# Kernel tuning notes

Hardware: AMD Instinct MI355X
Metric: run time of the kernel (lower is better)

## Reference

```python
import jax, jax.numpy as jnp
import numpy as np

LN_EPS = 1e-5


def _pos_embed_2d(w, h, c, dtype=jnp.float32):
    # matches build_2d_sincos_position_embedding: meshgrid indexing='xy' -> (h, w) grids
    grid_w = jnp.arange(w, dtype=jnp.float32)
    grid_h = jnp.arange(h, dtype=jnp.float32)
    gw, gh = jnp.meshgrid(grid_w, grid_h, indexing='xy')  # each (h, w)
    pos_dim = c // 4
    omega = 1.0 / (10000.0 ** (jnp.arange(pos_dim, dtype=jnp.float32) / pos_dim))
    out_w = gw.reshape(-1, 1) * omega[None]  # (h*w, pos_dim)
    out_h = gh.reshape(-1, 1) * omega[None]
    pe = jnp.concatenate([jnp.sin(out_w), jnp.cos(out_w), jnp.sin(out_h), jnp.cos(out_h)], axis=1)
    return pe.astype(dtype)  # (h*w, c)


def setup_inputs() -> dict:
    key = jax.random.key(0)
    k1, k2 = jax.random.split(key)
    N, C, H, W = 16, 256, 40, 40
    x = jax.random.normal(k1, (N, C, H, W), dtype=jnp.float32)
    ln_w = jnp.ones((C,), dtype=jnp.float32)
    ln_b = jnp.zeros((C,), dtype=jnp.float32)
    qkv_w = jax.random.normal(k2, (3 * C, C), dtype=jnp.float32) * 0.02  # 1x1 conv weight
    qkv_b = jnp.zeros((3 * C,), dtype=jnp.float32)
    gamma = jnp.ones((1,), dtype=jnp.float32)
    return {"x": x, "ln_w": ln_w, "ln_b": ln_b, "qkv_w": qkv_w, "qkv_b": qkv_b, "gamma": gamma}


def reference(x, ln_w, ln_b, qkv_w, qkv_b, gamma):
    N, C, H, W = x.shape
    scale = C ** (-0.5)
    identity = x

    # LayerNorm over channels (computed in NHWC like the torch permute dance)
    xh = jnp.transpose(x, (0, 2, 3, 1))  # (N, H, W, C)
    mu = jnp.mean(xh, axis=-1, keepdims=True)
    var = jnp.mean(jnp.square(xh - mu), axis=-1, keepdims=True)
    xn = (xh - mu) * jax.lax.rsqrt(var + LN_EPS) * ln_w + ln_b

    # 1x1 conv == per-pixel linear
    qkv = jnp.einsum('nhwc,oc->nhwo', xn, qkv_w) + qkv_b  # (N, H, W, 3C)
    qkv = qkv.reshape(N, H * W, 3 * C)
    q, k, v = jnp.split(qkv, 3, axis=-1)  # each (N, HW, C)

    pe = _pos_embed_2d(W, H, C, x.dtype)  # (HW, C)
    q = q + pe
    k = k + pe

    attn = jax.nn.softmax(jnp.einsum('nqc,nkc->nqk', q, k) * scale, axis=-1)
    out = jnp.einsum('nqk,nkc->nqc', attn, v)  # (N, HW, C)
    out = jnp.transpose(out, (0, 2, 1)).reshape(N, C, H, W)
    return identity + gamma[0] * out
```

## Files before the change

kernel.cpp:

```cpp
#include <hip/hip_runtime.h>
#include <hip/hip_bf16.h>

typedef float f32x4 __attribute__((ext_vector_type(4)));
typedef float f32x16 __attribute__((ext_vector_type(16)));
typedef __bf16 v8bf __attribute__((ext_vector_type(8)));
typedef unsigned short ushortx4 __attribute__((ext_vector_type(4)));
typedef unsigned short ushortx8 __attribute__((ext_vector_type(8)));
typedef unsigned int uint4v __attribute__((ext_vector_type(4)));

#define NIMG 16
#define CCH  256
#define HWP  1600
#define APIT 264

__device__ __forceinline__ unsigned short f2bf(float f) {
  unsigned int u = __builtin_bit_cast(unsigned int, f);
  u = (u + 0x7FFFu + ((u >> 16) & 1u)) >> 16;
  return (unsigned short)u;
}

__device__ __forceinline__ f32x4 mfma16(v8bf a, v8bf b, f32x4 c) {
  return __builtin_amdgcn_mfma_f32_16x16x32_bf16(a, b, c, 0, 0, 0);
}

__device__ __forceinline__ unsigned cvtpk(float a, float b) {
  unsigned r;
  asm("v_cvt_pk_bf16_f32 %0, %1, %2" : "=v"(r) : "v"(a), "v"(b));
  return r;
}
#define PSWAP(a, b) asm("v_permlane32_swap_b32 %0, %1" : "+v"(a), "+v"(b))

__global__ void prep_kernel(const float* __restrict__ qkv_w,
                            float* __restrict__ pe,
                            unsigned short* __restrict__ w_frag) {
  int tid = blockIdx.x * blockDim.x + threadIdx.x;
  int nthr = gridDim.x * blockDim.x;
  for (int i = tid; i < 768 * 256; i += nthr) {
    int o = i >> 8, c = i & 255;
    int tile = o >> 4, lr = o & 15;
    int ks = c >> 5, lg = (c >> 3) & 3, e = c & 7;
    w_frag[(((size_t)tile * 8 + ks) * 64 + lg * 16 + lr) * 8 + e] = f2bf(qkv_w[i]);
  }
  const float c1 = 9.210340371976184f / 64.f;
  for (int i = tid; i < HWP * 256; i += nthr) {
    int p = i >> 8, c = i & 255;
    int j = p % 40, ii = p / 40;
    int tt = c & 63;
    float omega = expf(-(float)tt * c1);
    float coord = (c < 128) ? (float)j : (float)ii;
    float a = coord * omega;
    pe[i] = ((c & 64) == 0) ? sinf(a) : cosf(a);
  }
}

__global__ __launch_bounds__(512, 4) void ln_qkv_kernel(
    const float* __restrict__ x, const float* __restrict__ ln_w, const float* __restrict__ ln_b,
    const unsigned short* __restrict__ w_frag, const float* __restrict__ qkv_b,
    const float* __restrict__ pe,
    unsigned short* __restrict__ q_arr, unsigned short* __restrict__ k_arr,
    unsigned short* __restrict__ v_arr) {
  __shared__ unsigned short buf[64][APIT];
  __shared__ float red_s[8][64], red_q[8][64];
  __shared__ float mu_s[64], rs_s[64];

  int t = threadIdx.x;
  int n = blockIdx.x / 25, pt = blockIdx.x % 25;
  int pix0 = pt * 64;
  int p = t & 63, g = t >> 6;
  const float* xb = x + (size_t)n * CCH * HWP + pix0;

  {
    float sum = 0.f, sq = 0.f;
#pragma unroll
    for (int i = 0; i < 32; ++i) {
      float v = xb[(size_t)(g * 32 + i) * HWP + p];
      sum += v; sq += v * v;
    }
    red_s[g][p] = sum; red_q[g][p] = sq;
  }
  __syncthreads();
  if (t < 64) {
    float s = 0.f, q2 = 0.f;
#pragma unroll
    for (int gg = 0; gg < 8; ++gg) { s += red_s[gg][t]; q2 += red_q[gg][t]; }
    float mu = s * (1.f / 256.f);
    float var = q2 * (1.f / 256.f) - mu * mu;
    mu_s[t] = mu;
    rs_s[t] = rsqrtf(var + 1e-5f);
  }
  __syncthreads();
  {
    float mu = mu_s[p], rs = rs_s[p];
#pragma unroll
    for (int i4 = 0; i4 < 8; ++i4) {
      int c0 = g * 32 + i4 * 4;
      f32x4 lw = *(const f32x4*)&ln_w[c0];
      f32x4 lb = *(const f32x4*)&ln_b[c0];
      ushortx4 pk;
#pragma unroll
      for (int r = 0; r < 4; ++r) {
        float v = xb[(size_t)(c0 + r) * HWP + p];
        pk[r] = f2bf((v - mu) * rs * lw[r] + lb[r]);
      }
      *(ushortx4*)&buf[p][c0] = pk;
    }
  }
  __syncthreads();

  int w = t >> 6, l = t & 63, lr = l & 15, lg = l >> 4;
  f32x4 acc[6][4];
#pragma unroll
  for (int nf = 0; nf < 6; ++nf)
#pragma unroll
    for (int mi = 0; mi < 4; ++mi) acc[nf][mi] = (f32x4){0.f, 0.f, 0.f, 0.f};

#pragma unroll
  for (int ks = 0; ks < 8; ++ks) {
    v8bf bF[4];
#pragma unroll
    for (int mi = 0; mi < 4; ++mi)
      bF[mi] = *(const v8bf*)&buf[mi * 16 + lr][ks * 32 + lg * 8];
#pragma unroll
    for (int nf = 0; nf < 6; ++nf) {
      int tile = w + nf * 8;
      v8bf wf = *(const v8bf*)&w_frag[(((size_t)tile * 8 + ks) * 64 + l) * 8];
#pragma unroll
      for (int mi = 0; mi < 4; ++mi) acc[nf][mi] = mfma16(wf, bF[mi], acc[nf][mi]);
    }
  }

  int lgh = lg >> 1, lgl = lg & 1;
#pragma unroll
  for (int nf = 0; nf < 2; ++nf) {
    int tile = w + nf * 8;
    f32x4 bi = *(const f32x4*)&qkv_b[tile * 16 + lg * 4];
#pragma unroll
    for (int mi = 0; mi < 4; ++mi) {
      int pix = pix0 + mi * 16 + lr;
      f32x4 pev = *(const f32x4*)&pe[(size_t)pix * 256 + tile * 16 + lg * 4];
      f32x4 vv = (acc[nf][mi] + bi + pev) * 0.0625f;
      ushortx4 pk = {f2bf(vv[0]), f2bf(vv[1]), f2bf(vv[2]), f2bf(vv[3])};
      int qt = pix >> 5, l31 = pix & 31;
      size_t ad = ((((size_t)n * 50 + qt) * 16 + tile) * 2 + lgh) * 256 + l31 * 8 + lgl * 4;
      *(ushortx4*)&q_arr[ad] = pk;
    }
  }
#pragma unroll
  for (int nf = 2; nf < 4; ++nf) {
    int tile = w + nf * 8;
    int dt = tile - 16;
    f32x4 bi = *(const f32x4*)&qkv_b[tile * 16 + lg * 4];
#pragma unroll
    for (int mi = 0; mi < 4; ++mi) {
      int pix = pix0 + mi * 16 + lr;
      f32x4 pev = *(const f32x4*)&pe[(size_t)pix * 256 + dt * 16 + lg * 4];
      f32x4 vv = acc[nf][mi] + bi + pev;
      ushortx4 pk = {f2bf(vv[0]), f2bf(vv[1]), f2bf(vv[2]), f2bf(vv[3])};
      size_t ad = (((size_t)n * 16 + dt) * 1600 + pix) * 16 + lgh * 8 + lgl * 4;
      *(ushortx4*)&k_arr[ad] = pk;
    }
  }
#pragma unroll
  for (int nf = 4; nf < 6; ++nf) {
    int tile = w + nf * 8;
    f32x4 bi = *(const f32x4*)&qkv_b[tile * 16 + lg * 4];
#pragma unroll
    for (int mi = 0; mi < 4; ++mi) {
      int pix = pix0 + mi * 16 + lr;
      int kvs = pix >> 4, hi = (pix >> 3) & 1, e = pix & 7;
      f32x4 vv = acc[nf][mi] + bi;
      size_t vb = (((size_t)n * 100 + kvs) * 2 + hi) * 2048 + e;
      int d0 = (tile - 32) * 16 + lg * 4;
#pragma unroll
      for (int r = 0; r < 4; ++r)
        v_arr[vb + (size_t)(d0 + r) * 8] = f2bf(vv[r]);
    }
  }
}

__global__ __launch_bounds__(256, 2) void attn_kernel(
    const unsigned short* __restrict__ q_arr, const unsigned short* __restrict__ k_arr,
    const unsigned short* __restrict__ v_arr, const float* __restrict__ x,
    const float* __restrict__ gamma, float* __restrict__ out) {
  __shared__ float sx[2][2][2][4][64][4];

  int t = threadIdx.x;
  int wv = t >> 6, l = t & 63;
  int l31 = l & 31, hi = l >> 5;
  int qsub = wv & 1, dh = wv >> 1;
  int dto = dh * 8;
  int dto32 = dh * 4;
  int slot = blockIdx.x & 7, j = blockIdx.x >> 3;
  int n = slot + 8 * (j / 25);
  int qb = j % 25;
  int qt = qb * 2 + qsub;
  int q0 = qt * 32;

  v8bf qf[8];
  {
    const unsigned short* qp = q_arr + (((size_t)n * 50 + qt) * 32 + hi) * 256 + l31 * 8;
#pragma unroll
    for (int i = 0; i < 8; ++i)
      qf[i] = *(const v8bf*)(qp + (dto + i) * 512);
  }

  f32x16 acc[4];
#pragma unroll
  for (int dd = 0; dd < 4; ++dd)
#pragma unroll
    for (int r = 0; r < 16; ++r) acc[dd][r] = 0.f;

  float m_run = -1e30f, l_run = 0.f;

  const unsigned short* kbase = k_arr + (size_t)n * (16 * 1600 * 16) +
                                (size_t)dto * 25600 + hi * 8;
  const unsigned short* vbase = v_arr + (size_t)n * (100 * 2 * 256 * 8) +
                                hi * 2048 + l31 * 8 + dto32 * 256;

  v8bf kc[8];
#pragma unroll
  for (int i = 0; i < 8; ++i)
    kc[i] = *(const v8bf*)(kbase + (size_t)i * 25600 + l31 * 16);

  for (int kt = 0; kt < 50; ++kt) {
    int pb = kt & 1;
    int ktn = (kt + 1 < 50) ? kt + 1 : 0;

    f32x16 s0, s1;
#pragma unroll
    for (int r = 0; r < 16; ++r) { s0[r] = 0.f; s1[r] = 0.f; }
#pragma unroll
    for (int i = 0; i < 8; i += 2) {
      s0 = __builtin_amdgcn_mfma_f32_32x32x16_bf16(kc[i], qf[i], s0, 0, 0, 0);
      s1 = __builtin_amdgcn_mfma_f32_32x32x16_bf16(kc[i + 1], qf[i + 1], s1, 0, 0, 0);
    }
#pragma unroll
    for (int i = 0; i < 8; ++i)
      kc[i] = *(const v8bf*)(kbase + (size_t)i * 25600 + (ktn * 32 + l31) * 16);

#pragma unroll
    for (int r4 = 0; r4 < 4; ++r4) {
      f32x4 vv = {s0[r4 * 4 + 0] + s1[r4 * 4 + 0], s0[r4 * 4 + 1] + s1[r4 * 4 + 1],
                  s0[r4 * 4 + 2] + s1[r4 * 4 + 2], s0[r4 * 4 + 3] + s1[r4 * 4 + 3]};
      *(f32x4*)&sx[qsub][pb][dh][r4][l][0] = vv;
    }

    v8bf vf0[4], vf1[4];
    {
      const unsigned short* vp = vbase + (size_t)kt * 8192;
#pragma unroll
      for (int i = 0; i < 4; ++i) vf0[i] = *(const v8bf*)(vp + i * 256);
#pragma unroll
      for (int i = 0; i < 4; ++i) vf1[i] = *(const v8bf*)(vp + 4096 + i * 256);
    }

    __syncthreads();

    float p[16];
#pragma unroll
    for (int r4 = 0; r4 < 4; ++r4) {
      f32x4 oth = *(const f32x4*)&sx[qsub][pb][dh ^ 1][r4][l][0];
#pragma unroll
      for (int rr = 0; rr < 4; ++rr)
        p[r4 * 4 + rr] = (s0[r4 * 4 + rr] + s1[r4 * 4 + rr]) + oth[rr];
    }

    float t0 = fmaxf(p[0], p[1]), t1 = fmaxf(p[2], p[3]);
    float t2 = fmaxf(p[4], p[5]), t3 = fmaxf(p[6], p[7]);
    float t4 = fmaxf(p[8], p[9]), t5 = fmaxf(p[10], p[11]);
    float t6 = fmaxf(p[12], p[13]), t7 = fmaxf(p[14], p[15]);
    float mx = fmaxf(fmaxf(fmaxf(t0, t1), fmaxf(t2, t3)),
                     fmaxf(fmaxf(t4, t5), fmaxf(t6, t7)));
    mx = fmaxf(mx, __shfl_xor(mx, 32));
    if (!__all(mx <= m_run + 2.f)) {
      float mnew = fmaxf(m_run, mx);
      float alpha = __expf(m_run - mnew);
      l_run *= alpha;
#pragma unroll
      for (int dd = 0; dd < 4; ++dd)
#pragma unroll
        for (int r = 0; r < 16; ++r) acc[dd][r] *= alpha;
      m_run = mnew;
    }
#pragma unroll
    for (int r = 0; r < 16; ++r) p[r] = __expf(p[r] - m_run);
    float sA = (p[0] + p[1]) + (p[2] + p[3]);
    float sB = (p[4] + p[5]) + (p[6] + p[7]);
    float sC = (p[8] + p[9]) + (p[10] + p[11]);
    float sD = (p[12] + p[13]) + (p[14] + p[15]);
    float sum = (sA + sB) + (sC + sD);
    sum += __shfl_xor(sum, 32);
    l_run += sum;

    unsigned x0 = cvtpk(p[0], p[1]), x1 = cvtpk(p[2], p[3]);
    unsigned y0 = cvtpk(p[4], p[5]), y1 = cvtpk(p[6], p[7]);
    PSWAP(x0, y0); PSWAP(x1, y1);
    uint4v u0 = {x0, x1, y0, y1};
    v8bf pf0 = __builtin_bit_cast(v8bf, u0);
    unsigned z0 = cvtpk(p[8], p[9]), z1 = cvtpk(p[10], p[11]);
    unsigned w0 = cvtpk(p[12], p[13]), w1 = cvtpk(p[14], p[15]);
    PSWAP(z0, w0); PSWAP(z1, w1);
    uint4v u1 = {z0, z1, w0, w1};
    v8bf pf1 = __builtin_bit_cast(v8bf, u1);

#pragma unroll
    for (int dd = 0; dd < 4; ++dd) {
      acc[dd] = __builtin_amdgcn_mfma_f32_32x32x16_bf16(vf0[dd], pf0, acc[dd], 0, 0, 0);
      acc[dd] = __builtin_amdgcn_mfma_f32_32x32x16_bf16(vf1[dd], pf1, acc[dd], 0, 0, 0);
    }
  }

  float inv = 1.f / l_run;
  float gm = gamma[0];
#pragma unroll
  for (int dd = 0; dd < 4; ++dd) {
#pragma unroll
    for (int r = 0; r < 16; ++r) {
      int d = (dto32 + dd) * 32 + (r & 3) + 8 * (r >> 2) + 4 * hi;
      size_t base = ((size_t)n * 256 + d) * HWP + q0 + l31;
      out[base] = x[base] + gm * acc[dd][r] * inv;
    }
  }
}

extern "C" void kernel_launch(void* const* d_in, const int* in_sizes, int n_in,
                              void* d_out, int out_size, void* d_ws, size_t ws_size,
                              hipStream_t stream) {
  const float* x     = (const float*)d_in[0];
  const float* ln_w  = (const float*)d_in[1];
  const float* ln_b  = (const float*)d_in[2];
  const float* qkv_w = (const float*)d_in[3];
  const float* qkv_b = (const float*)d_in[4];
  const float* gamma = (const float*)d_in[5];
  float* out = (float*)d_out;

  char* ws = (char*)d_ws;
  unsigned short* w_frag = (unsigned short*)ws;
  float*          pe     = (float*)(ws + 393216);
  unsigned short* q_arr  = (unsigned short*)(ws + 2031616);
  unsigned short* k_arr  = (unsigned short*)(ws + 15138816);
  unsigned short* v_arr  = (unsigned short*)(ws + 28246016);

  hipLaunchKernelGGL(prep_kernel, dim3(384), dim3(256), 0, stream, qkv_w, pe, w_frag);
  hipLaunchKernelGGL(ln_qkv_kernel, dim3(400), dim3(512), 0, stream,
                     x, ln_w, ln_b, w_frag, qkv_b, pe, q_arr, k_arr, v_arr);
  hipLaunchKernelGGL(attn_kernel, dim3(400), dim3(256), 0, stream,
                     q_arr, k_arr, v_arr, x, gamma, out);
}
```

Before: 133.0 us.

## Split attention KV range across wave pairs with flash-decoding style merge

Each attention block now handles one 32-query tile instead of two, with the two wave pairs processing disjoint halves of the key/value sequence. Partial softmax statistics and accumulators are merged through shared memory at the end. The grid doubles to 800 blocks to raise occupancy across the CUs. The cost is an extra LDS reduction and twice the Q fragment loads per query.

```diff
diff --git a/kernel.cpp b/kernel.cpp
--- a/kernel.cpp
+++ b/kernel.cpp
@@ -182,19 +182,20 @@
     const unsigned short* __restrict__ q_arr, const unsigned short* __restrict__ k_arr,
     const unsigned short* __restrict__ v_arr, const float* __restrict__ x,
     const float* __restrict__ gamma, float* __restrict__ out) {
-  __shared__ float sx[2][2][2][4][64][4];
+  __shared__ float pool[8192];
+  __shared__ float mls[4][2][32];
 
   int t = threadIdx.x;
   int wv = t >> 6, l = t & 63;
   int l31 = l & 31, hi = l >> 5;
-  int qsub = wv & 1, dh = wv >> 1;
+  int kvh = wv & 1, dh = wv >> 1;
   int dto = dh * 8;
   int dto32 = dh * 4;
   int slot = blockIdx.x & 7, j = blockIdx.x >> 3;
-  int n = slot + 8 * (j / 25);
-  int qb = j % 25;
-  int qt = qb * 2 + qsub;
+  int n = slot + 8 * (j / 50);
+  int qt = j % 50;
   int q0 = qt * 32;
+  int kt0 = kvh * 25;
 
   v8bf qf[8];
   {
@@ -220,11 +221,12 @@
   v8bf kc[8];
 #pragma unroll
   for (int i = 0; i < 8; ++i)
-    kc[i] = *(const v8bf*)(kbase + (size_t)i * 25600 + l31 * 16);
-
-  for (int kt = 0; kt < 50; ++kt) {
-    int pb = kt & 1;
-    int ktn = (kt + 1 < 50) ? kt + 1 : 0;
+    kc[i] = *(const v8bf*)(kbase + (size_t)i * 25600 + (kt0 * 32 + l31) * 16);
+
+  for (int it = 0; it < 25; ++it) {
+    int kt = kt0 + it;
+    int pb = it & 1;
+    int ktn = (it + 1 < 25) ? kt + 1 : kt0;
 
     f32x16 s0, s1;
 #pragma unroll
@@ -238,11 +240,12 @@
     for (int i = 0; i < 8; ++i)
       kc[i] = *(const v8bf*)(kbase + (size_t)i * 25600 + (ktn * 32 + l31) * 16);
 
+    int sxw = ((pb * 2 + kvh) * 2 + dh) * 1024;
 #pragma unroll
     for (int r4 = 0; r4 < 4; ++r4) {
       f32x4 vv = {s0[r4 * 4 + 0] + s1[r4 * 4 + 0], s0[r4 * 4 + 1] + s1[r4 * 4 + 1],
                   s0[r4 * 4 + 2] + s1[r4 * 4 + 2], s0[r4 * 4 + 3] + s1[r4 * 4 + 3]};
-      *(f32x4*)&sx[qsub][pb][dh][r4][l][0] = vv;
+      *(f32x4*)&pool[sxw + r4 * 256 + l * 4] = vv;
     }
 
     v8bf vf0[4], vf1[4];
@@ -256,10 +259,11 @@
 
     __syncthreads();
 
+    int sxr = ((pb * 2 + kvh) * 2 + (dh ^ 1)) * 1024;
     float p[16];
 #pragma unroll
     for (int r4 = 0; r4 < 4; ++r4) {
-      f32x4 oth = *(const f32x4*)&sx[qsub][pb][dh ^ 1][r4][l][0];
+      f32x4 oth = *(const f32x4*)&pool[sxr + r4 * 256 + l * 4];
 #pragma unroll
       for (int rr = 0; rr < 4; ++rr)
         p[r4 * 4 + rr] = (s0[r4 * 4 + rr] + s1[r4 * 4 + rr]) + oth[rr];
@@ -310,17 +314,55 @@
     }
   }
 
-  float inv = 1.f / l_run;
+  __syncthreads();
+  if (hi == 0) {
+    mls[kvh * 2 + dh][0][l31] = m_run;
+    mls[kvh * 2 + dh][1][l31] = l_run;
+  }
+  if (kvh == 0) {
+#pragma unroll
+    for (int r4 = 0; r4 < 4; ++r4) {
+      f32x4 a2 = {acc[2][r4 * 4 + 0], acc[2][r4 * 4 + 1], acc[2][r4 * 4 + 2], acc[2][r4 * 4 + 3]};
+      f32x4 a3 = {acc[3][r4 * 4 + 0], acc[3][r4 * 4 + 1], acc[3][r4 * 4 + 2], acc[3][r4 * 4 + 3]};
+      *(f32x4*)&pool[(((dh * 2 + 0) * 2 + 0) * 4 + r4) * 256 + l * 4] = a2;
+      *(f32x4*)&pool[(((dh * 2 + 0) * 2 + 1) * 4 + r4) * 256 + l * 4] = a3;
+    }
+  } else {
+#pragma unroll
+    for (int r4 = 0; r4 < 4; ++r4) {
+      f32x4 a0 = {acc[0][r4 * 4 + 0], acc[0][r4 * 4 + 1], acc[0][r4 * 4 + 2], acc[0][r4 * 4 + 3]};
+      f32x4 a1 = {acc[1][r4 * 4 + 0], acc[1][r4 * 4 + 1], acc[1][r4 * 4 + 2], acc[1][r4 * 4 + 3]};
+      *(f32x4*)&pool[(((dh * 2 + 1) * 2 + 0) * 4 + r4) * 256 + l * 4] = a0;
+      *(f32x4*)&pool[(((dh * 2 + 1) * 2 + 1) * 4 + r4) * 256 + l * 4] = a1;
+    }
+  }
+  __syncthreads();
+
+  float m_o = mls[(kvh ^ 1) * 2 + dh][0][l31];
+  float l_o = mls[(kvh ^ 1) * 2 + dh][1][l31];
+  float M = fmaxf(m_run, m_o);
+  float a_s = __expf(m_run - M), a_o = __expf(m_o - M);
+  float linv = 1.f / (l_run * a_s + l_o * a_o);
   float gm = gamma[0];
-#pragma unroll
-  for (int dd = 0; dd < 4; ++dd) {
-#pragma unroll
-    for (int r = 0; r < 16; ++r) {
-      int d = (dto32 + dd) * 32 + (r & 3) + 8 * (r >> 2) + 4 * hi;
-      size_t base = ((size_t)n * 256 + d) * HWP + q0 + l31;
-      out[base] = x[base] + gm * acc[dd][r] * inv;
-    }
-  }
+
+#define FIN(DT, PK, S)                                                          \
+  {                                                                             \
+    _Pragma("unroll")                                                           \
+    for (int r4 = 0; r4 < 4; ++r4) {                                            \
+      f32x4 oth = *(const f32x4*)&pool[(((dh * 2 + (PK)) * 2 + (S)) * 4 + r4) * 256 + l * 4]; \
+      _Pragma("unroll")                                                         \
+      for (int rr = 0; rr < 4; ++rr) {                                          \
+        int r = r4 * 4 + rr;                                                    \
+        float o = acc[DT][r] * a_s + oth[rr] * a_o;                             \
+        int d = (dto32 + (DT)) * 32 + (r & 3) + 8 * (r >> 2) + 4 * hi;          \
+        size_t base = ((size_t)n * 256 + d) * HWP + q0 + l31;                   \
+        out[base] = x[base] + gm * o * linv;                                    \
+      }                                                                         \
+    }                                                                           \
+  }
+  if (kvh == 0) { FIN(0, 1, 0); FIN(1, 1, 1); }
+  else          { FIN(2, 0, 0); FIN(3, 0, 1); }
+#undef FIN
 }
 
 extern "C" void kernel_launch(void* const* d_in, const int* in_sizes, int n_in,
@@ -344,6 +386,6 @@
   hipLaunchKernelGGL(prep_kernel, dim3(384), dim3(256), 0, stream, qkv_w, pe, w_frag);
   hipLaunchKernelGGL(ln_qkv_kernel, dim3(400), dim3(512), 0, stream,
                      x, ln_w, ln_b, w_frag, qkv_b, pe, q_arr, k_arr, v_arr);
-  hipLaunchKernelGGL(attn_kernel, dim3(400), dim3(256), 0, stream,
+  hipLaunchKernelGGL(attn_kernel, dim3(800), dim3(256), 0, stream,
                      q_arr, k_arr, v_arr, x, gamma, out);
 }
```

Result: no change. 135.6 us (+2.0%).

## Split attention into single-wave blocks, use exp2 softmax, stage V stores through LDS

Applied to the files above, without the earlier changes.

The attention kernel now gives each 64-thread block a full 256-dim QK^T dot product. The old version split the head dimension across waves and exchanged partial scores through shared memory with a barrier every key tile; that exchange is removed. Q is prescaled by log2(e)/16 so the softmax can use the raw v_exp_f32 instruction, and the rescale-deferral threshold is adjusted to match. The V output in the LN/QKV kernel is first transposed in LDS and then written with 16-byte stores instead of scattered 2-byte stores. The cost is twice the K and Q register footprint per wave, and each K tile is now loaded redundantly by two blocks.

```diff
diff --git a/kernel.cpp b/kernel.cpp
--- a/kernel.cpp
+++ b/kernel.cpp
@@ -13,6 +13,9 @@
 #define HWP  1600
 #define APIT 264
 
+#define QSCALE 0.09016844f
+#define DEFER_THR 2.885390f
+
 __device__ __forceinline__ unsigned short f2bf(float f) {
   unsigned int u = __builtin_bit_cast(unsigned int, f);
   u = (u + 0x7FFFu + ((u >> 16) & 1u)) >> 16;
@@ -26,6 +29,11 @@
 __device__ __forceinline__ unsigned cvtpk(float a, float b) {
   unsigned r;
   asm("v_cvt_pk_bf16_f32 %0, %1, %2" : "=v"(r) : "v"(a), "v"(b));
+  return r;
+}
+__device__ __forceinline__ float exp2v(float x) {
+  float r;
+  asm("v_exp_f32 %0, %1" : "=v"(r) : "v"(x));
   return r;
 }
 #define PSWAP(a, b) asm("v_permlane32_swap_b32 %0, %1" : "+v"(a), "+v"(b))
@@ -128,8 +136,22 @@
       for (int mi = 0; mi < 4; ++mi) acc[nf][mi] = mfma16(wf, bF[mi], acc[nf][mi]);
     }
   }
+  __syncthreads();
 
   int lgh = lg >> 1, lgl = lg & 1;
+#pragma unroll
+  for (int nf = 4; nf < 6; ++nf) {
+    int tile = w + nf * 8;
+    f32x4 bi = *(const f32x4*)&qkv_b[tile * 16 + lg * 4];
+    int d0 = (tile - 32) * 16 + lg * 4;
+#pragma unroll
+    for (int mi = 0; mi < 4; ++mi) {
+      int pixl = mi * 16 + lr;
+      f32x4 vv = acc[nf][mi] + bi;
+      ushortx4 pk = {f2bf(vv[0]), f2bf(vv[1]), f2bf(vv[2]), f2bf(vv[3])};
+      *(ushortx4*)&buf[pixl][d0] = pk;
+    }
+  }
 #pragma unroll
   for (int nf = 0; nf < 2; ++nf) {
     int tile = w + nf * 8;
@@ -138,7 +160,7 @@
     for (int mi = 0; mi < 4; ++mi) {
       int pix = pix0 + mi * 16 + lr;
       f32x4 pev = *(const f32x4*)&pe[(size_t)pix * 256 + tile * 16 + lg * 4];
-      f32x4 vv = (acc[nf][mi] + bi + pev) * 0.0625f;
+      f32x4 vv = (acc[nf][mi] + bi + pev) * QSCALE;
       ushortx4 pk = {f2bf(vv[0]), f2bf(vv[1]), f2bf(vv[2]), f2bf(vv[3])};
       int qt = pix >> 5, l31 = pix & 31;
       size_t ad = ((((size_t)n * 50 + qt) * 16 + tile) * 2 + lgh) * 256 + l31 * 8 + lgl * 4;
@@ -160,48 +182,39 @@
       *(ushortx4*)&k_arr[ad] = pk;
     }
   }
-#pragma unroll
-  for (int nf = 4; nf < 6; ++nf) {
-    int tile = w + nf * 8;
-    f32x4 bi = *(const f32x4*)&qkv_b[tile * 16 + lg * 4];
-#pragma unroll
-    for (int mi = 0; mi < 4; ++mi) {
-      int pix = pix0 + mi * 16 + lr;
-      int kvs = pix >> 4, hi = (pix >> 3) & 1, e = pix & 7;
-      f32x4 vv = acc[nf][mi] + bi;
-      size_t vb = (((size_t)n * 100 + kvs) * 2 + hi) * 2048 + e;
-      int d0 = (tile - 32) * 16 + lg * 4;
-#pragma unroll
-      for (int r = 0; r < 4; ++r)
-        v_arr[vb + (size_t)(d0 + r) * 8] = f2bf(vv[r]);
-    }
-  }
-}
-
-__global__ __launch_bounds__(256, 2) void attn_kernel(
+  __syncthreads();
+#pragma unroll
+  for (int it = 0; it < 4; ++it) {
+    int u = t + it * 512;
+    int kvsl = u >> 9, hi2 = (u >> 8) & 1, d = u & 255;
+    ushortx8 vv;
+#pragma unroll
+    for (int e = 0; e < 8; ++e) vv[e] = buf[kvsl * 16 + hi2 * 8 + e][d];
+    size_t di = (((size_t)n * 100 + pt * 4 + kvsl) * 2 + hi2) * 256 + d;
+    *(ushortx8*)&v_arr[di * 8] = vv;
+  }
+}
+
+__global__ __launch_bounds__(64, 2) void attn_kernel(
     const unsigned short* __restrict__ q_arr, const unsigned short* __restrict__ k_arr,
     const unsigned short* __restrict__ v_arr, const float* __restrict__ x,
     const float* __restrict__ gamma, float* __restrict__ out) {
-  __shared__ float sx[2][2][2][4][64][4];
-
-  int t = threadIdx.x;
-  int wv = t >> 6, l = t & 63;
+  int l = threadIdx.x;
   int l31 = l & 31, hi = l >> 5;
-  int qsub = wv & 1, dh = wv >> 1;
-  int dto = dh * 8;
+  int slot = blockIdx.x & 7, j = blockIdx.x >> 3;
+  int n = slot + 8 * (j / 100);
+  int rem = j % 100;
+  int qt = rem >> 1;
+  int dh = rem & 1;
+  int q0 = qt * 32;
   int dto32 = dh * 4;
-  int slot = blockIdx.x & 7, j = blockIdx.x >> 3;
-  int n = slot + 8 * (j / 25);
-  int qb = j % 25;
-  int qt = qb * 2 + qsub;
-  int q0 = qt * 32;
-
-  v8bf qf[8];
+
+  v8bf qf[16];
   {
     const unsigned short* qp = q_arr + (((size_t)n * 50 + qt) * 32 + hi) * 256 + l31 * 8;
 #pragma unroll
-    for (int i = 0; i < 8; ++i)
-      qf[i] = *(const v8bf*)(qp + (dto + i) * 512);
+    for (int i = 0; i < 16; ++i)
+      qf[i] = *(const v8bf*)(qp + i * 512);
   }
 
   f32x16 acc[4];
@@ -212,59 +225,33 @@
 
   float m_run = -1e30f, l_run = 0.f;
 
-  const unsigned short* kbase = k_arr + (size_t)n * (16 * 1600 * 16) +
-                                (size_t)dto * 25600 + hi * 8;
+  const unsigned short* kbase = k_arr + (size_t)n * (16 * 1600 * 16) + hi * 8;
   const unsigned short* vbase = v_arr + (size_t)n * (100 * 2 * 256 * 8) +
                                 hi * 2048 + l31 * 8 + dto32 * 256;
 
-  v8bf kc[8];
-#pragma unroll
-  for (int i = 0; i < 8; ++i)
+  v8bf kc[16];
+#pragma unroll
+  for (int i = 0; i < 16; ++i)
     kc[i] = *(const v8bf*)(kbase + (size_t)i * 25600 + l31 * 16);
 
   for (int kt = 0; kt < 50; ++kt) {
-    int pb = kt & 1;
     int ktn = (kt + 1 < 50) ? kt + 1 : 0;
 
     f32x16 s0, s1;
 #pragma unroll
     for (int r = 0; r < 16; ++r) { s0[r] = 0.f; s1[r] = 0.f; }
 #pragma unroll
-    for (int i = 0; i < 8; i += 2) {
+    for (int i = 0; i < 16; i += 2) {
       s0 = __builtin_amdgcn_mfma_f32_32x32x16_bf16(kc[i], qf[i], s0, 0, 0, 0);
       s1 = __builtin_amdgcn_mfma_f32_32x32x16_bf16(kc[i + 1], qf[i + 1], s1, 0, 0, 0);
     }
 #pragma unroll
-    for (int i = 0; i < 8; ++i)
+    for (int i = 0; i < 16; ++i)
       kc[i] = *(const v8bf*)(kbase + (size_t)i * 25600 + (ktn * 32 + l31) * 16);
 
-#pragma unroll
-    for (int r4 = 0; r4 < 4; ++r4) {
-      f32x4 vv = {s0[r4 * 4 + 0] + s1[r4 * 4 + 0], s0[r4 * 4 + 1] + s1[r4 * 4 + 1],
-                  s0[r4 * 4 + 2] + s1[r4 * 4 + 2], s0[r4 * 4 + 3] + s1[r4 * 4 + 3]};
-      *(f32x4*)&sx[qsub][pb][dh][r4][l][0] = vv;
-    }
-
-    v8bf vf0[4], vf1[4];
-    {
-      const unsigned short* vp = vbase + (size_t)kt * 8192;
-#pragma unroll
-      for (int i = 0; i < 4; ++i) vf0[i] = *(const v8bf*)(vp + i * 256);
-#pragma unroll
-      for (int i = 0; i < 4; ++i) vf1[i] = *(const v8bf*)(vp + 4096 + i * 256);
-    }
-
-    __syncthreads();
-
     float p[16];
 #pragma unroll
-    for (int r4 = 0; r4 < 4; ++r4) {
-      f32x4 oth = *(const f32x4*)&sx[qsub][pb][dh ^ 1][r4][l][0];
-#pragma unroll
-      for (int rr = 0; rr < 4; ++rr)
-        p[r4 * 4 + rr] = (s0[r4 * 4 + rr] + s1[r4 * 4 + rr]) + oth[rr];
-    }
-
+    for (int r = 0; r < 16; ++r) p[r] = s0[r] + s1[r];
     float t0 = fmaxf(p[0], p[1]), t1 = fmaxf(p[2], p[3]);
     float t2 = fmaxf(p[4], p[5]), t3 = fmaxf(p[6], p[7]);
     float t4 = fmaxf(p[8], p[9]), t5 = fmaxf(p[10], p[11]);
@@ -272,9 +259,17 @@
     float mx = fmaxf(fmaxf(fmaxf(t0, t1), fmaxf(t2, t3)),
                      fmaxf(fmaxf(t4, t5), fmaxf(t6, t7)));
     mx = fmaxf(mx, __shfl_xor(mx, 32));
-    if (!__all(mx <= m_run + 2.f)) {
+
+    v8bf vf0[4];
+    {
+      const unsigned short* vp = vbase + (size_t)kt * 8192;
+#pragma unroll
+      for (int i = 0; i < 4; ++i) vf0[i] = *(const v8bf*)(vp + i * 256);
+    }
+
+    if (!__all(mx <= m_run + DEFER_THR)) {
       float mnew = fmaxf(m_run, mx);
-      float alpha = __expf(m_run - mnew);
+      float alpha = exp2v(m_run - mnew);
       l_run *= alpha;
 #pragma unroll
       for (int dd = 0; dd < 4; ++dd)
@@ -283,14 +278,11 @@
       m_run = mnew;
     }
 #pragma unroll
-    for (int r = 0; r < 16; ++r) p[r] = __expf(p[r] - m_run);
-    float sA = (p[0] + p[1]) + (p[2] + p[3]);
-    float sB = (p[4] + p[5]) + (p[6] + p[7]);
-    float sC = (p[8] + p[9]) + (p[10] + p[11]);
-    float sD = (p[12] + p[13]) + (p[14] + p[15]);
-    float sum = (sA + sB) + (sC + sD);
-    sum += __shfl_xor(sum, 32);
-    l_run += sum;
+    for (int r = 0; r < 16; ++r) p[r] = exp2v(p[r] - m_run);
+    float sSum = ((p[0] + p[1]) + (p[2] + p[3])) + ((p[4] + p[5]) + (p[6] + p[7])) +
+                 (((p[8] + p[9]) + (p[10] + p[11])) + ((p[12] + p[13]) + (p[14] + p[15])));
+    sSum += __shfl_xor(sSum, 32);
+    l_run += sSum;
 
     unsigned x0 = cvtpk(p[0], p[1]), x1 = cvtpk(p[2], p[3]);
     unsigned y0 = cvtpk(p[4], p[5]), y1 = cvtpk(p[6], p[7]);
@@ -303,11 +295,19 @@
     uint4v u1 = {z0, z1, w0, w1};
     v8bf pf1 = __builtin_bit_cast(v8bf, u1);
 
-#pragma unroll
-    for (int dd = 0; dd < 4; ++dd) {
+    v8bf vf1[4];
+    {
+      const unsigned short* vp = vbase + (size_t)kt * 8192 + 4096;
+#pragma unroll
+      for (int i = 0; i < 4; ++i) vf1[i] = *(const v8bf*)(vp + i * 256);
+    }
+
+#pragma unroll
+    for (int dd = 0; dd < 4; ++dd)
       acc[dd] = __builtin_amdgcn_mfma_f32_32x32x16_bf16(vf0[dd], pf0, acc[dd], 0, 0, 0);
+#pragma unroll
+    for (int dd = 0; dd < 4; ++dd)
       acc[dd] = __builtin_amdgcn_mfma_f32_32x32x16_bf16(vf1[dd], pf1, acc[dd], 0, 0, 0);
-    }
   }
 
   float inv = 1.f / l_run;
@@ -344,6 +344,6 @@
   hipLaunchKernelGGL(prep_kernel, dim3(384), dim3(256), 0, stream, qkv_w, pe, w_frag);
   hipLaunchKernelGGL(ln_qkv_kernel, dim3(400), dim3(512), 0, stream,
                      x, ln_w, ln_b, w_frag, qkv_b, pe, q_arr, k_arr, v_arr);
-  hipLaunchKernelGGL(attn_kernel, dim3(400), dim3(256), 0, stream,
+  hipLaunchKernelGGL(attn_kernel, dim3(1600), dim3(64), 0, stream,
                      q_arr, k_arr, v_arr, x, gamma, out);
 }
```

Result: slower. 154.7 us (+16.3%).
